# Kernel optimization log

Measured on AMD Instinct MI355X. Metric: run time of the kernel, lower is better.

Reference implementation:

```python
import jax, jax.numpy as jnp
import numpy as np


def setup_inputs() -> dict:
    key = jax.random.key(0)
    k1, k2 = jax.random.split(key)
    query = jax.random.normal(k1, (32, 1, 1024), dtype=jnp.float32)
    keys = jax.random.normal(k2, (32, 4096, 1024), dtype=jnp.float32)
    return {"query": query, "keys": keys}


def reference(query, keys):
    # scores: (B, S) = keys (B,S,H) @ query (B,H,1), no 1/sqrt(d) scaling (faithful to source)
    scores = jnp.einsum("bsh,bh->bs", keys, query[:, 0, :])
    attention_weights = jax.nn.softmax(scores, axis=1)  # (B, S)
    # context: weighted sum of keys (module uses keys as values)
    context_vector = jnp.einsum("bs,bsh->bh", attention_weights, keys)  # (B, H)
    return (context_vector, attention_weights)
```

## Files before the change

### kernel.cpp

```cpp
#include <hip/hip_runtime.h>
#include <stdint.h>

#define BATCH 32
#define S 4096
#define H 1024
#define H4 (H / 4)
#define NCHUNK 16
#define KPC (S / NCHUNK)
#define BLOCK 256
#define NWAVE (BLOCK / 64)
#define TROWS 8
#define NTILES (KPC / TROWS)
#define RPW (TROWS / NWAVE)

typedef float vfloat4 __attribute__((ext_vector_type(4)));

__global__ __launch_bounds__(BLOCK) void attn_pass1(
    const float* __restrict__ query, const float* __restrict__ keys,
    float* __restrict__ scores,
    float* __restrict__ po,
    float* __restrict__ pm,
    float* __restrict__ pl)
{
  const int chunk = blockIdx.x;
  const int b     = blockIdx.y;
  const int lane  = threadIdx.x & 63;
  const int wave  = threadIdx.x >> 6;

  __shared__ __align__(16) float buf[2][TROWS][H];
  __shared__ float lds_m[NWAVE], lds_l[NWAVE];

  const vfloat4* q4 = (const vfloat4*)(query + (size_t)b * H);
  const vfloat4 q0 = q4[lane], q1 = q4[lane + 64], q2 = q4[lane + 128], q3 = q4[lane + 192];

  const float* kb = keys + ((size_t)b * S + (size_t)chunk * KPC) * (size_t)H;

  auto stage = [&](int t, int pb) {
    #pragma unroll
    for (int r = 0; r < RPW; ++r) {
      const int row = wave * RPW + r;
      const float* g = kb + (size_t)(t * TROWS + row) * H + lane * 4;
      #pragma unroll
      for (int qo = 0; qo < 4; ++qo) {
        __builtin_amdgcn_global_load_lds(
            (const __attribute__((address_space(1))) uint32_t*)(g + qo * 256),
            (__attribute__((address_space(3))) uint32_t*)(&buf[pb][row][qo * 256]),
            16, 0, 0);
      }
    }
  };

  float m = -3.0e38f, l = 0.0f;
  vfloat4 o0 = {0,0,0,0}, o1 = {0,0,0,0}, o2 = {0,0,0,0}, o3 = {0,0,0,0};

  stage(0, 0);
  __syncthreads();

  int pb = 0;
  for (int t = 0; t < NTILES; ++t) {
    if (t + 1 < NTILES) stage(t + 1, pb ^ 1);

    #pragma unroll
    for (int r = 0; r < RPW; ++r) {
      const int row = wave * RPW + r;
      const vfloat4* lrow = (const vfloat4*)&buf[pb][row][0];
      const vfloat4 k0 = lrow[lane],       k1 = lrow[lane + 64],
                    k2 = lrow[lane + 128], k3 = lrow[lane + 192];

      float d0 = k0.x*q0.x + k0.y*q0.y + k0.z*q0.z + k0.w*q0.w;
      float d1 = k1.x*q1.x + k1.y*q1.y + k1.z*q1.z + k1.w*q1.w;
      float d2 = k2.x*q2.x + k2.y*q2.y + k2.z*q2.z + k2.w*q2.w;
      float d3 = k3.x*q3.x + k3.y*q3.y + k3.z*q3.z + k3.w*q3.w;
      float d  = (d0 + d1) + (d2 + d3);
      #pragma unroll
      for (int off = 1; off < 64; off <<= 1) d += __shfl_xor(d, off);

      if (lane == 0) scores[(size_t)b * S + chunk * KPC + t * TROWS + row] = d;

      const float mn = fmaxf(m, d);
      const float sc = __expf(m - mn);
      const float p  = __expf(d - mn);
      l  = l * sc + p;
      o0 = o0*sc + p*k0;
      o1 = o1*sc + p*k1;
      o2 = o2*sc + p*k2;
      o3 = o3*sc + p*k3;
      m = mn;
    }

    __syncthreads();
    pb ^= 1;
  }

  float* red = &buf[0][0][0];
  vfloat4* lo = (vfloat4*)(red + wave * H);
  lo[lane] = o0; lo[lane + 64] = o1; lo[lane + 128] = o2; lo[lane + 192] = o3;
  if (lane == 0) { lds_m[wave] = m; lds_l[wave] = l; }
  __syncthreads();

  const int tid = threadIdx.x;
  const float bm = fmaxf(fmaxf(lds_m[0], lds_m[1]), fmaxf(lds_m[2], lds_m[3]));
  float bl = 0.0f;
  vfloat4 acc = {0,0,0,0};
  #pragma unroll
  for (int w = 0; w < NWAVE; ++w) {
    const float scw = __expf(lds_m[w] - bm);
    bl += lds_l[w] * scw;
    const vfloat4 ow = ((const vfloat4*)(red + w * H))[tid];
    acc += ow * scw;
  }
  ((vfloat4*)po)[((size_t)b * NCHUNK + chunk) * H4 + tid] = acc;
  if (tid == 0) { pm[b * NCHUNK + chunk] = bm; pl[b * NCHUNK + chunk] = bl; }
}

__global__ __launch_bounds__(256) void attn_pass2(
    const float* __restrict__ po, const float* __restrict__ pm, const float* __restrict__ pl,
    float* __restrict__ ctx, float* __restrict__ wts)
{
  const int b = blockIdx.x;
  const int t = threadIdx.x;
  __shared__ float s_scale[NCHUNK];
  __shared__ float s_m, s_invl;
  if (t == 0) {
    float m = -3.0e38f;
    for (int j = 0; j < NCHUNK; ++j) m = fmaxf(m, pm[b * NCHUNK + j]);
    float l = 0.0f;
    for (int j = 0; j < NCHUNK; ++j) {
      const float sc = __expf(pm[b * NCHUNK + j] - m);
      s_scale[j] = sc;
      l += pl[b * NCHUNK + j] * sc;
    }
    s_m = m; s_invl = 1.0f / l;
  }
  __syncthreads();
  const float m = s_m, invl = s_invl;

  vfloat4 acc = {0,0,0,0};
  for (int j = 0; j < NCHUNK; ++j) {
    const vfloat4 ow = ((const vfloat4*)po)[((size_t)b * NCHUNK + j) * H4 + t];
    acc += ow * s_scale[j];
  }
  acc *= invl;
  ((vfloat4*)ctx)[(size_t)b * H4 + t] = acc;

  for (int s = t; s < S; s += 256) {
    const float sc = wts[(size_t)b * S + s];
    wts[(size_t)b * S + s] = __expf(sc - m) * invl;
  }
}

extern "C" void kernel_launch(void* const* d_in, const int* in_sizes, int n_in,
                              void* d_out, int out_size, void* d_ws, size_t ws_size,
                              hipStream_t stream) {
  const float* query = (const float*)d_in[0];
  const float* keys  = (const float*)d_in[1];

  float* ctx = (float*)d_out;
  float* wts = (float*)d_out + BATCH * H;

  float* po = (float*)d_ws;
  float* pm = po + (size_t)BATCH * NCHUNK * H;
  float* pl = pm + BATCH * NCHUNK;

  attn_pass1<<<dim3(NCHUNK, BATCH), BLOCK, 0, stream>>>(query, keys, wts, po, pm, pl);
  attn_pass2<<<BATCH, 256, 0, stream>>>(po, pm, pl, ctx, wts);
}
```

Measured before the change: 684.3 us.

## Replace block-synchronized double buffer with per-wave 4-slot async load ring

Each wave now owns a contiguous range of 64 key rows and streams them through its own 4-slot LDS ring with three rows in flight. It waits on vmcnt counts instead of block-wide __syncthreads every tile. Scores are gathered in a register per lane and written with one coalesced store instead of a lane-0 store per row. The softmax normalization in pass2 is vectorized to float4. This removes block barriers and deepens memory prefetch, but relies on hand-tuned waitcnt values that must match the number of outstanding loads.

```diff
diff --git a/kernel.cpp b/kernel.cpp
--- a/kernel.cpp
+++ b/kernel.cpp
@@ -9,11 +9,13 @@
 #define KPC (S / NCHUNK)
 #define BLOCK 256
 #define NWAVE (BLOCK / 64)
-#define TROWS 8
-#define NTILES (KPC / TROWS)
-#define RPW (TROWS / NWAVE)
+#define KPW (KPC / NWAVE)
+#define NSLOT 4
 
 typedef float vfloat4 __attribute__((ext_vector_type(4)));
+
+#define WAITV(N) do { asm volatile("s_waitcnt vmcnt(" #N ")" ::: "memory"); \
+                      __builtin_amdgcn_sched_barrier(0); } while (0)
 
 __global__ __launch_bounds__(BLOCK) void attn_pass1(
     const float* __restrict__ query, const float* __restrict__ keys,
@@ -27,72 +29,72 @@
   const int lane  = threadIdx.x & 63;
   const int wave  = threadIdx.x >> 6;
 
-  __shared__ __align__(16) float buf[2][TROWS][H];
+  __shared__ __align__(16) float ring[NWAVE][NSLOT][H];
   __shared__ float lds_m[NWAVE], lds_l[NWAVE];
 
   const vfloat4* q4 = (const vfloat4*)(query + (size_t)b * H);
   const vfloat4 q0 = q4[lane], q1 = q4[lane + 64], q2 = q4[lane + 128], q3 = q4[lane + 192];
 
-  const float* kb = keys + ((size_t)b * S + (size_t)chunk * KPC) * (size_t)H;
+  const float* wbase = keys + ((size_t)b * S + (size_t)chunk * KPC + (size_t)wave * KPW) * (size_t)H;
 
-  auto stage = [&](int t, int pb) {
+  auto stage = [&](int r, int sl) {
+    const float* g = wbase + (size_t)r * H + lane * 4;
     #pragma unroll
-    for (int r = 0; r < RPW; ++r) {
-      const int row = wave * RPW + r;
-      const float* g = kb + (size_t)(t * TROWS + row) * H + lane * 4;
-      #pragma unroll
-      for (int qo = 0; qo < 4; ++qo) {
-        __builtin_amdgcn_global_load_lds(
-            (const __attribute__((address_space(1))) uint32_t*)(g + qo * 256),
-            (__attribute__((address_space(3))) uint32_t*)(&buf[pb][row][qo * 256]),
-            16, 0, 0);
-      }
+    for (int qo = 0; qo < 4; ++qo) {
+      __builtin_amdgcn_global_load_lds(
+          (const __attribute__((address_space(1))) uint32_t*)(g + qo * 256),
+          (__attribute__((address_space(3))) uint32_t*)(&ring[wave][sl][qo * 256]),
+          16, 0, 0);
     }
   };
 
-  float m = -3.0e38f, l = 0.0f;
+  stage(0, 0); __builtin_amdgcn_sched_barrier(0);
+  stage(1, 1); __builtin_amdgcn_sched_barrier(0);
+  stage(2, 2); __builtin_amdgcn_sched_barrier(0);
+
+  float m = -3.0e38f, l = 0.0f, sreg = 0.0f;
   vfloat4 o0 = {0,0,0,0}, o1 = {0,0,0,0}, o2 = {0,0,0,0}, o3 = {0,0,0,0};
 
-  stage(0, 0);
+  auto body = [&](int i) {
+    const vfloat4* lrow = (const vfloat4*)&ring[wave][i & (NSLOT - 1)][0];
+    const vfloat4 k0 = lrow[lane],       k1 = lrow[lane + 64],
+                  k2 = lrow[lane + 128], k3 = lrow[lane + 192];
+
+    float d0 = k0.x*q0.x + k0.y*q0.y + k0.z*q0.z + k0.w*q0.w;
+    float d1 = k1.x*q1.x + k1.y*q1.y + k1.z*q1.z + k1.w*q1.w;
+    float d2 = k2.x*q2.x + k2.y*q2.y + k2.z*q2.z + k2.w*q2.w;
+    float d3 = k3.x*q3.x + k3.y*q3.y + k3.z*q3.z + k3.w*q3.w;
+    float d  = (d0 + d1) + (d2 + d3);
+    #pragma unroll
+    for (int off = 1; off < 64; off <<= 1) d += __shfl_xor(d, off);
+
+    sreg = (lane == i) ? d : sreg;
+
+    const float mn = fmaxf(m, d);
+    const float sc = __expf(m - mn);
+    const float p  = __expf(d - mn);
+    l  = l * sc + p;
+    o0 = o0*sc + p*k0;
+    o1 = o1*sc + p*k1;
+    o2 = o2*sc + p*k2;
+    o3 = o3*sc + p*k3;
+    m = mn;
+  };
+
+  #pragma unroll 2
+  for (int i = 0; i < KPW - 3; ++i) {
+    stage(i + 3, (i + 3) & (NSLOT - 1));
+    WAITV(12);
+    body(i);
+  }
+  WAITV(8);  body(KPW - 3);
+  WAITV(4);  body(KPW - 2);
+  WAITV(0);  body(KPW - 1);
+
+  scores[(size_t)b * S + (size_t)chunk * KPC + (size_t)wave * KPW + lane] = sreg;
+
   __syncthreads();
-
-  int pb = 0;
-  for (int t = 0; t < NTILES; ++t) {
-    if (t + 1 < NTILES) stage(t + 1, pb ^ 1);
-
-    #pragma unroll
-    for (int r = 0; r < RPW; ++r) {
-      const int row = wave * RPW + r;
-      const vfloat4* lrow = (const vfloat4*)&buf[pb][row][0];
-      const vfloat4 k0 = lrow[lane],       k1 = lrow[lane + 64],
-                    k2 = lrow[lane + 128], k3 = lrow[lane + 192];
-
-      float d0 = k0.x*q0.x + k0.y*q0.y + k0.z*q0.z + k0.w*q0.w;
-      float d1 = k1.x*q1.x + k1.y*q1.y + k1.z*q1.z + k1.w*q1.w;
-      float d2 = k2.x*q2.x + k2.y*q2.y + k2.z*q2.z + k2.w*q2.w;
-      float d3 = k3.x*q3.x + k3.y*q3.y + k3.z*q3.z + k3.w*q3.w;
-      float d  = (d0 + d1) + (d2 + d3);
-      #pragma unroll
-      for (int off = 1; off < 64; off <<= 1) d += __shfl_xor(d, off);
-
-      if (lane == 0) scores[(size_t)b * S + chunk * KPC + t * TROWS + row] = d;
-
-      const float mn = fmaxf(m, d);
-      const float sc = __expf(m - mn);
-      const float p  = __expf(d - mn);
-      l  = l * sc + p;
-      o0 = o0*sc + p*k0;
-      o1 = o1*sc + p*k1;
-      o2 = o2*sc + p*k2;
-      o3 = o3*sc + p*k3;
-      m = mn;
-    }
-
-    __syncthreads();
-    pb ^= 1;
-  }
-
-  float* red = &buf[0][0][0];
+  float* red = &ring[0][0][0];
   vfloat4* lo = (vfloat4*)(red + wave * H);
   lo[lane] = o0; lo[lane + 64] = o1; lo[lane + 128] = o2; lo[lane + 192] = o3;
   if (lane == 0) { lds_m[wave] = m; lds_l[wave] = l; }
@@ -143,9 +145,14 @@
   acc *= invl;
   ((vfloat4*)ctx)[(size_t)b * H4 + t] = acc;
 
-  for (int s = t; s < S; s += 256) {
-    const float sc = wts[(size_t)b * S + s];
-    wts[(size_t)b * S + s] = __expf(sc - m) * invl;
+  vfloat4* w4 = (vfloat4*)(wts + (size_t)b * S);
+  for (int s = t; s < S / 4; s += 256) {
+    vfloat4 v = w4[s];
+    v.x = __expf(v.x - m) * invl;
+    v.y = __expf(v.y - m) * invl;
+    v.z = __expf(v.z - m) * invl;
+    v.w = __expf(v.w - m) * invl;
+    w4[s] = v;
   }
 }
 
```

Measured after the change: 683.4 us. Within noise of the previous version (-0.1%).
